# Optimization experiments

Hardware: AMD Instinct MI355X
Metric: run time of the kernel (lower is better)

The kernel has to match this reference:

```python
import jax, jax.numpy as jnp
import numpy as np

OUT_F, IN_F = 11008, 4096  # LLaMA-7B up-projection


def setup_inputs() -> dict:
    key = jax.random.key(0)
    k1, k2, k3, k4 = jax.random.split(key, 4)
    x = jax.random.normal(k1, (2, 512, IN_F), dtype=jnp.float32)
    # decoded int8 weights, stored as int32 per spec but valued in [-127, 127]
    weight_int8 = jax.random.randint(k2, (OUT_F, IN_F), -127, 128, dtype=jnp.int32)
    scale = jax.random.uniform(k3, (1,), dtype=jnp.float32) * 0.02 + 1e-3
    bias = jax.random.normal(k4, (OUT_F,), dtype=jnp.float32)
    return {"x": x, "weight_int8": weight_int8, "scale": scale, "bias": bias}


def reference(x, weight_int8, scale, bias):
    # dequantize: int8 * per-tensor scale  (done fresh every forward in original)
    weight = weight_int8.astype(jnp.float32) * scale[0]  # [out, in]
    # F.linear: x @ W^T + b
    out = jnp.einsum('bsi,oi->bso', x, weight) + bias
    return out
```

## Files before the change

kernel.cpp:

```cpp
#include <hip/hip_runtime.h>
#include <hip/hip_bf16.h>


#define M_TOT 1024
#define N_TOT 11008
#define K_TOT 4096
#define BM 256
#define BN 256
#define BKI 128
#define NTI (K_TOT / BKI)
#define ABYTES (BM * BKI)
#define BUFB   ((BM + BN) * BKI)

typedef __attribute__((ext_vector_type(8))) short short8;
typedef __attribute__((ext_vector_type(4))) float f32x4;
typedef __attribute__((ext_vector_type(4))) int   i32x4;

__device__ __forceinline__ unsigned short f2bf(float f) {
    __hip_bfloat16 h = __float2bfloat16(f);
    return __builtin_bit_cast(unsigned short, h);
}

__device__ __forceinline__ void gload16(const void* g, void* l) {
    __builtin_amdgcn_global_load_lds(
        (const __attribute__((address_space(1))) unsigned int*)g,
        (__attribute__((address_space(3))) unsigned int*)l,
        16, 0, 0);
}

__global__ void wpack_kernel(const int* __restrict__ W, int* __restrict__ Wq, int n16) {
    int idx = blockIdx.x * blockDim.x + threadIdx.x;
    int stride = gridDim.x * blockDim.x;
    for (int i = idx; i < n16; i += stride) {
        const int4* p = (const int4*)W + (size_t)i * 4;
        i32x4 o;
#pragma unroll
        for (int j = 0; j < 4; ++j) {
            int4 v = p[j];
            o[j] = (v.x & 0xff) | ((v.y & 0xff) << 8) | ((v.z & 0xff) << 16) | (v.w << 24);
        }
        *(i32x4*)(Wq + (size_t)i * 4) = o;
    }
}

__global__ __launch_bounds__(256)
void xquant_kernel(const float* __restrict__ X, int* __restrict__ Xq,
                   float* __restrict__ sx) {
    const int r = blockIdx.x;
    const int t = threadIdx.x;
    const float* xr = X + (size_t)r * K_TOT + t * 16;
    f32x4 v[4];
    float amax = 0.0f;
#pragma unroll
    for (int j = 0; j < 4; ++j) {
        v[j] = *(const f32x4*)(xr + j * 4);
#pragma unroll
        for (int e = 0; e < 4; ++e) amax = fmaxf(amax, fabsf(v[j][e]));
    }
#pragma unroll
    for (int k = 1; k < 64; k <<= 1) amax = fmaxf(amax, __shfl_xor(amax, k));
    __shared__ float sm[4];
    if ((t & 63) == 0) sm[t >> 6] = amax;
    __syncthreads();
    amax = fmaxf(fmaxf(sm[0], sm[1]), fmaxf(sm[2], sm[3]));
    const float inv = (amax > 0.0f) ? (127.0f / amax) : 0.0f;
    if (t == 0) sx[r] = (amax > 0.0f) ? (amax / 127.0f) : 0.0f;
    i32x4 o;
#pragma unroll
    for (int j = 0; j < 4; ++j) {
        int q[4];
#pragma unroll
        for (int e = 0; e < 4; ++e) {
            int qi = (int)rintf(v[j][e] * inv);
            qi = qi > 127 ? 127 : (qi < -127 ? -127 : qi);
            q[e] = qi;
        }
        o[j] = (q[0] & 0xff) | ((q[1] & 0xff) << 8) | ((q[2] & 0xff) << 16) | (q[3] << 24);
    }
    *(i32x4*)(Xq + (size_t)r * (K_TOT / 4) + t * 4) = o;
}

__global__ __launch_bounds__(512, 2)
void gemm_i8_kernel(const char* __restrict__ Xq,
                    const char* __restrict__ Wq,
                    const float* __restrict__ sx,
                    const float* __restrict__ scale,
                    const float* __restrict__ bias,
                    float* __restrict__ out) {
    __shared__ __align__(16) unsigned char lds[2 * BUFB];

    const int tid  = threadIdx.x;
    const int lane = tid & 63;
    const int wid  = tid >> 6;
    const int wr   = wid >> 2;
    const int wc   = wid & 3;
    const int lr   = lane & 15;
    const int kb   = lane >> 4;

    const int brow = blockIdx.y * BM;
    const int bcol = blockIdx.x * BN;

    const int s_row  = wid * 32 + (lane >> 3);
    const int s_colb = (((lane & 7) ^ (lane >> 3)) * 16);

    const char* asrc0 = Xq + (size_t)(brow + s_row) * K_TOT + s_colb;
    const char* bsrc0 = Wq + (size_t)(bcol + s_row) * K_TOT + s_colb;
    const int lds_row0 = wid * 32;

    auto stageA = [&](int t, unsigned char* buf) {
        const size_t k0 = (size_t)t * BKI;
#pragma unroll
        for (int i = 0; i < 4; ++i)
            gload16(asrc0 + k0 + (size_t)i * 8 * K_TOT, buf + (lds_row0 + i * 8) * BKI);
    };
    auto stageB = [&](int t, unsigned char* buf) {
        const size_t k0 = (size_t)t * BKI;
#pragma unroll
        for (int i = 0; i < 4; ++i)
            gload16(bsrc0 + k0 + (size_t)i * 8 * K_TOT, buf + ABYTES + (lds_row0 + i * 8) * BKI);
    };

    i32x4 acc[8][4];
#pragma unroll
    for (int m = 0; m < 8; ++m)
#pragma unroll
        for (int n = 0; n < 4; ++n)
#pragma unroll
            for (int i = 0; i < 4; ++i) acc[m][n][i] = 0;

    auto do_tile = [&](const unsigned char* cur, unsigned char* nxt, int tn) {
        stageA(tn, nxt);
        asm volatile("s_waitcnt vmcnt(4)" ::: "memory");
        __builtin_amdgcn_s_barrier();
        __builtin_amdgcn_sched_barrier(0);

        i32x4 a0[4], a1[4], a2[4], a3[4], b0[4], b1[4];
        const int c0 = (kb * 16);
        const int c1 = (64 + kb * 16);

#pragma unroll
        for (int n = 0; n < 4; ++n) {
            int row = wc * 64 + n * 16 + lr;
            b0[n] = *(const i32x4*)(cur + ABYTES + row * BKI + (c0 ^ ((row & 7) << 4)));
        }
#pragma unroll
        for (int m = 0; m < 4; ++m) {
            int row = wr * 128 + m * 16 + lr;
            a0[m] = *(const i32x4*)(cur + row * BKI + (c0 ^ ((row & 7) << 4)));
        }
#pragma unroll
        for (int m = 0; m < 4; ++m) {
            int row = wr * 128 + 64 + m * 16 + lr;
            a1[m] = *(const i32x4*)(cur + row * BKI + (c0 ^ ((row & 7) << 4)));
        }

        __builtin_amdgcn_s_setprio(1);
#pragma unroll
        for (int m = 0; m < 4; ++m)
#pragma unroll
            for (int n = 0; n < 4; ++n)
                acc[m][n] = __builtin_amdgcn_mfma_i32_16x16x64_i8(a0[m], b0[n], acc[m][n], 0, 0, 0);
        __builtin_amdgcn_s_setprio(0);

#pragma unroll
        for (int n = 0; n < 4; ++n) {
            int row = wc * 64 + n * 16 + lr;
            b1[n] = *(const i32x4*)(cur + ABYTES + row * BKI + (c1 ^ ((row & 7) << 4)));
        }
#pragma unroll
        for (int m = 0; m < 4; ++m) {
            int row = wr * 128 + m * 16 + lr;
            a2[m] = *(const i32x4*)(cur + row * BKI + (c1 ^ ((row & 7) << 4)));
        }

        __builtin_amdgcn_s_setprio(1);
#pragma unroll
        for (int m = 0; m < 4; ++m)
#pragma unroll
            for (int n = 0; n < 4; ++n)
                acc[4 + m][n] = __builtin_amdgcn_mfma_i32_16x16x64_i8(a1[m], b0[n], acc[4 + m][n], 0, 0, 0);
        __builtin_amdgcn_s_setprio(0);

#pragma unroll
        for (int m = 0; m < 4; ++m) {
            int row = wr * 128 + 64 + m * 16 + lr;
            a3[m] = *(const i32x4*)(cur + row * BKI + (c1 ^ ((row & 7) << 4)));
        }
        stageB(tn, nxt);

        __builtin_amdgcn_s_setprio(1);
#pragma unroll
        for (int m = 0; m < 4; ++m)
#pragma unroll
            for (int n = 0; n < 4; ++n)
                acc[m][n] = __builtin_amdgcn_mfma_i32_16x16x64_i8(a2[m], b1[n], acc[m][n], 0, 0, 0);
        __builtin_amdgcn_s_setprio(0);

        __builtin_amdgcn_s_setprio(1);
#pragma unroll
        for (int m = 0; m < 4; ++m)
#pragma unroll
            for (int n = 0; n < 4; ++n)
                acc[4 + m][n] = __builtin_amdgcn_mfma_i32_16x16x64_i8(a3[m], b1[n], acc[4 + m][n], 0, 0, 0);
        __builtin_amdgcn_s_setprio(0);

        asm volatile("s_waitcnt lgkmcnt(0)" ::: "memory");
        __builtin_amdgcn_s_barrier();
    };

    unsigned char* buf0 = lds;
    unsigned char* buf1 = lds + BUFB;

    stageA(0, buf0);
    stageB(0, buf0);

    for (int t = 0; t < NTI; t += 2) {
        do_tile(buf0, buf1, t + 1);
        do_tile(buf1, buf0, (t + 2 < NTI) ? t + 2 : 0);
    }

    const float sw = scale[0];
    const int orow0 = brow + wr * 128;
    const int ocol0 = bcol + wc * 64;
    float bv[4];
#pragma unroll
    for (int n = 0; n < 4; ++n) bv[n] = bias[ocol0 + n * 16 + lr];
#pragma unroll
    for (int m = 0; m < 8; ++m) {
        f32x4 sx4 = *(const f32x4*)(sx + orow0 + m * 16 + kb * 4);
#pragma unroll
        for (int i = 0; i < 4; ++i) {
            int r = orow0 + m * 16 + kb * 4 + i;
            size_t base = (size_t)r * N_TOT + ocol0;
            float fs = sx4[i] * sw;
#pragma unroll
            for (int n = 0; n < 4; ++n)
                out[base + n * 16 + lr] = (float)acc[m][n][i] * fs + bv[n];
        }
    }
}

__device__ __forceinline__ unsigned long long pack4(float a, float b, float c, float d) {
    return (unsigned long long)f2bf(a)
         | ((unsigned long long)f2bf(b) << 16)
         | ((unsigned long long)f2bf(c) << 32)
         | ((unsigned long long)f2bf(d) << 48);
}

#define FBM 128
#define FBN 128
#define FBK 64
#define FNT (K_TOT / FBK)

__global__ __launch_bounds__(256, 2)
void otf_linear_fused(const float* __restrict__ X, const int* __restrict__ W,
                      const float* __restrict__ scale, const float* __restrict__ bias,
                      float* __restrict__ out) {
    __shared__ __align__(16) unsigned char AsB[FBM * FBK * 2];
    __shared__ __align__(16) unsigned char BsB[FBN * FBK * 2];

    const int tid = threadIdx.x, lane = tid & 63, wid = tid >> 6;
    const int wr = wid >> 1, wc = wid & 1, lr = lane & 15, kb = lane >> 4;
    const int brow = blockIdx.y * FBM, bcol = blockIdx.x * FBN;
    const int srow = tid >> 4, sc4 = tid & 15;

    f32x4 areg[8];
    int4 breg[8];
    auto load_tiles = [&](int t) {
        const int k0 = t * FBK;
#pragma unroll
        for (int p = 0; p < 8; ++p) {
            int row = p * 16 + srow;
            areg[p] = *(const f32x4*)(&X[(size_t)(brow + row) * K_TOT + k0 + sc4 * 4]);
            breg[p] = *(const int4*)(&W[(size_t)(bcol + row) * K_TOT + k0 + sc4 * 4]);
        }
    };
    auto store_tiles = [&]() {
#pragma unroll
        for (int p = 0; p < 8; ++p) {
            int row = p * 16 + srow;
            int boff = (sc4 * 8) ^ ((row & 7) << 4);
            *(unsigned long long*)(&AsB[row * 128 + boff]) =
                pack4(areg[p][0], areg[p][1], areg[p][2], areg[p][3]);
            *(unsigned long long*)(&BsB[row * 128 + boff]) =
                pack4((float)breg[p].x, (float)breg[p].y, (float)breg[p].z, (float)breg[p].w);
        }
    };

    f32x4 acc[4][4];
#pragma unroll
    for (int m = 0; m < 4; ++m)
#pragma unroll
        for (int n = 0; n < 4; ++n)
#pragma unroll
            for (int i = 0; i < 4; ++i) acc[m][n][i] = 0.0f;

    load_tiles(0);
    for (int t = 0; t < FNT; ++t) {
        store_tiles();
        __syncthreads();
        if (t + 1 < FNT) load_tiles(t + 1);
#pragma unroll
        for (int kk = 0; kk < 2; ++kk) {
            short8 af[4], bfr[4];
#pragma unroll
            for (int m = 0; m < 4; ++m) {
                int row = wr * 64 + m * 16 + lr;
                int col = (kk * 64 + kb * 16) ^ ((row & 7) << 4);
                af[m] = *(const short8*)(&AsB[row * 128 + col]);
            }
#pragma unroll
            for (int n = 0; n < 4; ++n) {
                int row = wc * 64 + n * 16 + lr;
                int col = (kk * 64 + kb * 16) ^ ((row & 7) << 4);
                bfr[n] = *(const short8*)(&BsB[row * 128 + col]);
            }
#pragma unroll
            for (int m = 0; m < 4; ++m)
#pragma unroll
                for (int n = 0; n < 4; ++n)
                    acc[m][n] = __builtin_amdgcn_mfma_f32_16x16x32_bf16(af[m], bfr[n], acc[m][n], 0, 0, 0);
        }
        __syncthreads();
    }

    const float sc = scale[0];
    const int orow0 = brow + wr * 64, ocol0 = bcol + wc * 64;
    float bv[4];
#pragma unroll
    for (int n = 0; n < 4; ++n) bv[n] = bias[ocol0 + n * 16 + lr];
#pragma unroll
    for (int m = 0; m < 4; ++m)
#pragma unroll
        for (int i = 0; i < 4; ++i) {
            int r = orow0 + m * 16 + kb * 4 + i;
            size_t base = (size_t)r * N_TOT + ocol0;
#pragma unroll
            for (int n = 0; n < 4; ++n)
                out[base + n * 16 + lr] = acc[m][n][i] * sc + bv[n];
        }
}

extern "C" void kernel_launch(void* const* d_in, const int* in_sizes, int n_in,
                              void* d_out, int out_size, void* d_ws, size_t ws_size,
                              hipStream_t stream) {
    const float* x     = (const float*)d_in[0];
    const int*   w     = (const int*)d_in[1];
    const float* scale = (const float*)d_in[2];
    const float* bias  = (const float*)d_in[3];
    float* out = (float*)d_out;

    const size_t W_ELEMS = (size_t)N_TOT * K_TOT;
    const size_t X_ELEMS = (size_t)M_TOT * K_TOT;
    const size_t need = W_ELEMS + X_ELEMS + M_TOT * sizeof(float);

    if (ws_size >= need) {
        char*  Wq = (char*)d_ws;
        char*  Xq = (char*)d_ws + W_ELEMS;
        float* sx = (float*)((char*)d_ws + W_ELEMS + X_ELEMS);
        wpack_kernel<<<2048, 256, 0, stream>>>(w, (int*)Wq, (int)(W_ELEMS / 16));
        xquant_kernel<<<M_TOT, 256, 0, stream>>>(x, (int*)Xq, sx);
        gemm_i8_kernel<<<dim3(N_TOT / BN, M_TOT / BM), 512, 0, stream>>>(
            Xq, Wq, sx, scale, bias, out);
    } else {
        otf_linear_fused<<<dim3(N_TOT / FBN, M_TOT / FBM), 256, 0, stream>>>(x, w, scale, bias, out);
    }
}
```

Before: 96.48 us.

## Fuse int32 weight packing into the int8 GEMM with smaller tiles and XCD swizzle

Removes the separate weight-packing pass that converted the int32 weights to int8 in workspace. The GEMM now loads raw int32 weight rows into registers, packs them to int8 and writes them to LDS inside the K-loop, alongside the async LDS loads for the quantized activations. Tiles shrink from 256x256 to 128x128 with 256 threads, and a 1D grid is remapped so that blocks sharing a weight column tile land on the same XCD for L2 reuse. This saves a full read and write of the weights in an extra kernel, but the GEMM now reads four times as many weight bytes per tile. It also waits on all vector loads every tile, which may expose global-load latency.

```diff
diff --git a/kernel.cpp b/kernel.cpp
--- a/kernel.cpp
+++ b/kernel.cpp
@@ -5,12 +5,12 @@
 #define M_TOT 1024
 #define N_TOT 11008
 #define K_TOT 4096
-#define BM 256
-#define BN 256
+#define BM 128
+#define BN 128
 #define BKI 128
 #define NTI (K_TOT / BKI)
-#define ABYTES (BM * BKI)
-#define BUFB   ((BM + BN) * BKI)
+#define ABYTES_ (BM * BKI)
+#define BUFB    ((BM + BN) * BKI)
 
 typedef __attribute__((ext_vector_type(8))) short short8;
 typedef __attribute__((ext_vector_type(4))) float f32x4;
@@ -26,21 +26,6 @@
         (const __attribute__((address_space(1))) unsigned int*)g,
         (__attribute__((address_space(3))) unsigned int*)l,
         16, 0, 0);
-}
-
-__global__ void wpack_kernel(const int* __restrict__ W, int* __restrict__ Wq, int n16) {
-    int idx = blockIdx.x * blockDim.x + threadIdx.x;
-    int stride = gridDim.x * blockDim.x;
-    for (int i = idx; i < n16; i += stride) {
-        const int4* p = (const int4*)W + (size_t)i * 4;
-        i32x4 o;
-#pragma unroll
-        for (int j = 0; j < 4; ++j) {
-            int4 v = p[j];
-            o[j] = (v.x & 0xff) | ((v.y & 0xff) << 8) | ((v.z & 0xff) << 16) | (v.w << 24);
-        }
-        *(i32x4*)(Wq + (size_t)i * 4) = o;
-    }
 }
 
 __global__ __launch_bounds__(256)
@@ -80,32 +65,33 @@
     *(i32x4*)(Xq + (size_t)r * (K_TOT / 4) + t * 4) = o;
 }
 
-__global__ __launch_bounds__(512, 2)
-void gemm_i8_kernel(const char* __restrict__ Xq,
-                    const char* __restrict__ Wq,
-                    const float* __restrict__ sx,
-                    const float* __restrict__ scale,
-                    const float* __restrict__ bias,
-                    float* __restrict__ out) {
+__global__ __launch_bounds__(256, 2)
+void gemm_fused_kernel(const char* __restrict__ Xq,
+                       const int* __restrict__ W,
+                       const float* __restrict__ sx,
+                       const float* __restrict__ scale,
+                       const float* __restrict__ bias,
+                       float* __restrict__ out) {
     __shared__ __align__(16) unsigned char lds[2 * BUFB];
 
     const int tid  = threadIdx.x;
     const int lane = tid & 63;
     const int wid  = tid >> 6;
-    const int wr   = wid >> 2;
-    const int wc   = wid & 3;
+    const int wr   = wid >> 1;
+    const int wc   = wid & 1;
     const int lr   = lane & 15;
     const int kb   = lane >> 4;
 
-    const int brow = blockIdx.y * BM;
-    const int bcol = blockIdx.x * BN;
-
-    const int s_row  = wid * 32 + (lane >> 3);
-    const int s_colb = (((lane & 7) ^ (lane >> 3)) * 16);
+    const int orig = blockIdx.x;
+    const int wg   = (orig & 7) * 86 + (orig >> 3);
+    const int brow = (wg & 7) * BM;
+    const int bcol = (wg >> 3) * BN;
+
+    const int lds_row0 = wid * 32;
+    const int s_row  = lds_row0 + (lane >> 3);
+    const int s_colb = ((lane & 7) ^ (lane >> 3)) * 16;
 
     const char* asrc0 = Xq + (size_t)(brow + s_row) * K_TOT + s_colb;
-    const char* bsrc0 = Wq + (size_t)(bcol + s_row) * K_TOT + s_colb;
-    const int lds_row0 = wid * 32;
 
     auto stageA = [&](int t, unsigned char* buf) {
         const size_t k0 = (size_t)t * BKI;
@@ -113,47 +99,70 @@
         for (int i = 0; i < 4; ++i)
             gload16(asrc0 + k0 + (size_t)i * 8 * K_TOT, buf + (lds_row0 + i * 8) * BKI);
     };
-    auto stageB = [&](int t, unsigned char* buf) {
-        const size_t k0 = (size_t)t * BKI;
+
+    const int* bW[4];
+#pragma unroll
+    for (int i = 0; i < 4; ++i)
+        bW[i] = W + (size_t)(bcol + lds_row0 + i * 8 + (lane >> 3)) * K_TOT + (lane & 7) * 16;
+
+    auto packw = [&](const int4 q[4]) {
+        i32x4 o;
+#pragma unroll
+        for (int j = 0; j < 4; ++j)
+            o[j] = (q[j].x & 0xff) | ((q[j].y & 0xff) << 8) |
+                   ((q[j].z & 0xff) << 16) | (q[j].w << 24);
+        return o;
+    };
+    auto bwrite = [&](unsigned char* buf, int i, i32x4 v) {
+        *(i32x4*)(buf + ABYTES_ + (lds_row0 + i * 8 + (lane >> 3)) * BKI + s_colb) = v;
+    };
+
+    i32x4 acc[4][4];
+#pragma unroll
+    for (int m = 0; m < 4; ++m)
+#pragma unroll
+        for (int n = 0; n < 4; ++n)
+#pragma unroll
+            for (int i = 0; i < 4; ++i) acc[m][n][i] = 0;
+
+    unsigned char* buf0 = lds;
+    unsigned char* buf1 = lds + BUFB;
+
+    {
+        int4 bq[4][4];
 #pragma unroll
         for (int i = 0; i < 4; ++i)
-            gload16(bsrc0 + k0 + (size_t)i * 8 * K_TOT, buf + ABYTES + (lds_row0 + i * 8) * BKI);
-    };
-
-    i32x4 acc[8][4];
-#pragma unroll
-    for (int m = 0; m < 8; ++m)
-#pragma unroll
-        for (int n = 0; n < 4; ++n)
-#pragma unroll
-            for (int i = 0; i < 4; ++i) acc[m][n][i] = 0;
+#pragma unroll
+            for (int j = 0; j < 4; ++j)
+                bq[i][j] = *(const int4*)(bW[i] + j * 4);
+        stageA(0, buf0);
+#pragma unroll
+        for (int i = 0; i < 4; ++i) bwrite(buf0, i, packw(bq[i]));
+        asm volatile("s_waitcnt vmcnt(0) lgkmcnt(0)" ::: "memory");
+        __builtin_amdgcn_s_barrier();
+    }
 
     auto do_tile = [&](const unsigned char* cur, unsigned char* nxt, int tn) {
+        int4 bq[4][4];
+#pragma unroll
+        for (int i = 0; i < 4; ++i)
+#pragma unroll
+            for (int j = 0; j < 4; ++j)
+                bq[i][j] = *(const int4*)(bW[i] + tn * BKI + j * 4);
         stageA(tn, nxt);
-        asm volatile("s_waitcnt vmcnt(4)" ::: "memory");
-        __builtin_amdgcn_s_barrier();
         __builtin_amdgcn_sched_barrier(0);
 
-        i32x4 a0[4], a1[4], a2[4], a3[4], b0[4], b1[4];
-        const int c0 = (kb * 16);
-        const int c1 = (64 + kb * 16);
-
+        i32x4 a0[4], b0[4], a1[4], b1[4];
 #pragma unroll
         for (int n = 0; n < 4; ++n) {
             int row = wc * 64 + n * 16 + lr;
-            b0[n] = *(const i32x4*)(cur + ABYTES + row * BKI + (c0 ^ ((row & 7) << 4)));
+            b0[n] = *(const i32x4*)(cur + ABYTES_ + row * BKI + ((kb * 16) ^ ((row & 7) << 4)));
         }
 #pragma unroll
         for (int m = 0; m < 4; ++m) {
-            int row = wr * 128 + m * 16 + lr;
-            a0[m] = *(const i32x4*)(cur + row * BKI + (c0 ^ ((row & 7) << 4)));
-        }
-#pragma unroll
-        for (int m = 0; m < 4; ++m) {
-            int row = wr * 128 + 64 + m * 16 + lr;
-            a1[m] = *(const i32x4*)(cur + row * BKI + (c0 ^ ((row & 7) << 4)));
-        }
-
+            int row = wr * 64 + m * 16 + lr;
+            a0[m] = *(const i32x4*)(cur + row * BKI + ((kb * 16) ^ ((row & 7) << 4)));
+        }
         __builtin_amdgcn_s_setprio(1);
 #pragma unroll
         for (int m = 0; m < 4; ++m)
@@ -161,58 +170,35 @@
             for (int n = 0; n < 4; ++n)
                 acc[m][n] = __builtin_amdgcn_mfma_i32_16x16x64_i8(a0[m], b0[n], acc[m][n], 0, 0, 0);
         __builtin_amdgcn_s_setprio(0);
+        __builtin_amdgcn_sched_barrier(0);
+
+        bwrite(nxt, 0, packw(bq[0]));
+        bwrite(nxt, 1, packw(bq[1]));
 
 #pragma unroll
         for (int n = 0; n < 4; ++n) {
             int row = wc * 64 + n * 16 + lr;
-            b1[n] = *(const i32x4*)(cur + ABYTES + row * BKI + (c1 ^ ((row & 7) << 4)));
+            b1[n] = *(const i32x4*)(cur + ABYTES_ + row * BKI + ((64 + kb * 16) ^ ((row & 7) << 4)));
         }
 #pragma unroll
         for (int m = 0; m < 4; ++m) {
-            int row = wr * 128 + m * 16 + lr;
-            a2[m] = *(const i32x4*)(cur + row * BKI + (c1 ^ ((row & 7) << 4)));
-        }
-
+            int row = wr * 64 + m * 16 + lr;
+            a1[m] = *(const i32x4*)(cur + row * BKI + ((64 + kb * 16) ^ ((row & 7) << 4)));
+        }
         __builtin_amdgcn_s_setprio(1);
 #pragma unroll
         for (int m = 0; m < 4; ++m)
 #pragma unroll
             for (int n = 0; n < 4; ++n)
-                acc[4 + m][n] = __builtin_amdgcn_mfma_i32_16x16x64_i8(a1[m], b0[n], acc[4 + m][n], 0, 0, 0);
+                acc[m][n] = __builtin_amdgcn_mfma_i32_16x16x64_i8(a1[m], b1[n], acc[m][n], 0, 0, 0);
         __builtin_amdgcn_s_setprio(0);
 
-#pragma unroll
-        for (int m = 0; m < 4; ++m) {
-            int row = wr * 128 + 64 + m * 16 + lr;
-            a3[m] = *(const i32x4*)(cur + row * BKI + (c1 ^ ((row & 7) << 4)));
-        }
-        stageB(tn, nxt);
-
-        __builtin_amdgcn_s_setprio(1);
-#pragma unroll
-        for (int m = 0; m < 4; ++m)
-#pragma unroll
-            for (int n = 0; n < 4; ++n)
-                acc[m][n] = __builtin_amdgcn_mfma_i32_16x16x64_i8(a2[m], b1[n], acc[m][n], 0, 0, 0);
-        __builtin_amdgcn_s_setprio(0);
-
-        __builtin_amdgcn_s_setprio(1);
-#pragma unroll
-        for (int m = 0; m < 4; ++m)
-#pragma unroll
-            for (int n = 0; n < 4; ++n)
-                acc[4 + m][n] = __builtin_amdgcn_mfma_i32_16x16x64_i8(a3[m], b1[n], acc[4 + m][n], 0, 0, 0);
-        __builtin_amdgcn_s_setprio(0);
-
-        asm volatile("s_waitcnt lgkmcnt(0)" ::: "memory");
+        bwrite(nxt, 2, packw(bq[2]));
+        bwrite(nxt, 3, packw(bq[3]));
+
+        asm volatile("s_waitcnt vmcnt(0) lgkmcnt(0)" ::: "memory");
         __builtin_amdgcn_s_barrier();
     };
-
-    unsigned char* buf0 = lds;
-    unsigned char* buf1 = lds + BUFB;
-
-    stageA(0, buf0);
-    stageB(0, buf0);
 
     for (int t = 0; t < NTI; t += 2) {
         do_tile(buf0, buf1, t + 1);
@@ -220,13 +206,13 @@
     }
 
     const float sw = scale[0];
-    const int orow0 = brow + wr * 128;
+    const int orow0 = brow + wr * 64;
     const int ocol0 = bcol + wc * 64;
     float bv[4];
 #pragma unroll
     for (int n = 0; n < 4; ++n) bv[n] = bias[ocol0 + n * 16 + lr];
 #pragma unroll
-    for (int m = 0; m < 8; ++m) {
+    for (int m = 0; m < 4; ++m) {
         f32x4 sx4 = *(const f32x4*)(sx + orow0 + m * 16 + kb * 4);
 #pragma unroll
         for (int i = 0; i < 4; ++i) {
@@ -350,18 +336,14 @@
     const float* bias  = (const float*)d_in[3];
     float* out = (float*)d_out;
 
-    const size_t W_ELEMS = (size_t)N_TOT * K_TOT;
     const size_t X_ELEMS = (size_t)M_TOT * K_TOT;
-    const size_t need = W_ELEMS + X_ELEMS + M_TOT * sizeof(float);
+    const size_t need = X_ELEMS + M_TOT * sizeof(float);
 
     if (ws_size >= need) {
-        char*  Wq = (char*)d_ws;
-        char*  Xq = (char*)d_ws + W_ELEMS;
-        float* sx = (float*)((char*)d_ws + W_ELEMS + X_ELEMS);
-        wpack_kernel<<<2048, 256, 0, stream>>>(w, (int*)Wq, (int)(W_ELEMS / 16));
+        char*  Xq = (char*)d_ws;
+        float* sx = (float*)((char*)d_ws + X_ELEMS);
         xquant_kernel<<<M_TOT, 256, 0, stream>>>(x, (int*)Xq, sx);
-        gemm_i8_kernel<<<dim3(N_TOT / BN, M_TOT / BM), 512, 0, stream>>>(
-            Xq, Wq, sx, scale, bias, out);
+        gemm_fused_kernel<<<dim3(688), 256, 0, stream>>>(Xq, w, sx, scale, bias, out);
     } else {
         otf_linear_fused<<<dim3(N_TOT / FBN, M_TOT / FBM), 256, 0, stream>>>(x, w, scale, bias, out);
     }
```

Result: slower. 156.4 us (+62.1%).

## Fuse int32-to-int8 weight packing into the GEMM B-tile staging

Applied to the files above, without the earlier changes.

Removes the separate weight-packing kernel and its int8 workspace. The GEMM now reads the int32 weights straight from global memory into registers, packs them to int8 and writes them into the swizzled LDS B tile. The loads and packs are interleaved with the MFMA phases, and the end-of-tile wait now also covers outstanding global loads. This drops a full extra pass over the weights. In exchange, each row-block reads the 4-byte weights rather than packed bytes, which quadruples weight traffic unless the caches absorb it. It also adds register pressure and a less asynchronous B path.

```diff
diff --git a/kernel.cpp b/kernel.cpp
--- a/kernel.cpp
+++ b/kernel.cpp
@@ -28,19 +28,8 @@
         16, 0, 0);
 }
 
-__global__ void wpack_kernel(const int* __restrict__ W, int* __restrict__ Wq, int n16) {
-    int idx = blockIdx.x * blockDim.x + threadIdx.x;
-    int stride = gridDim.x * blockDim.x;
-    for (int i = idx; i < n16; i += stride) {
-        const int4* p = (const int4*)W + (size_t)i * 4;
-        i32x4 o;
-#pragma unroll
-        for (int j = 0; j < 4; ++j) {
-            int4 v = p[j];
-            o[j] = (v.x & 0xff) | ((v.y & 0xff) << 8) | ((v.z & 0xff) << 16) | (v.w << 24);
-        }
-        *(i32x4*)(Wq + (size_t)i * 4) = o;
-    }
+__device__ __forceinline__ int packb(int4 v) {
+    return (v.x & 0xff) | ((v.y & 0xff) << 8) | ((v.z & 0xff) << 16) | (v.w << 24);
 }
 
 __global__ __launch_bounds__(256)
@@ -81,8 +70,8 @@
 }
 
 __global__ __launch_bounds__(512, 2)
-void gemm_i8_kernel(const char* __restrict__ Xq,
-                    const char* __restrict__ Wq,
+void gemm_fw_kernel(const char* __restrict__ Xq,
+                    const int* __restrict__ W,
                     const float* __restrict__ sx,
                     const float* __restrict__ scale,
                     const float* __restrict__ bias,
@@ -99,13 +88,11 @@
 
     const int brow = blockIdx.y * BM;
     const int bcol = blockIdx.x * BN;
-
-    const int s_row  = wid * 32 + (lane >> 3);
+    const int lds_row0 = wid * 32;
+
+    const int s_row  = lds_row0 + (lane >> 3);
     const int s_colb = (((lane & 7) ^ (lane >> 3)) * 16);
-
     const char* asrc0 = Xq + (size_t)(brow + s_row) * K_TOT + s_colb;
-    const char* bsrc0 = Wq + (size_t)(bcol + s_row) * K_TOT + s_colb;
-    const int lds_row0 = wid * 32;
 
     auto stageA = [&](int t, unsigned char* buf) {
         const size_t k0 = (size_t)t * BKI;
@@ -113,11 +100,26 @@
         for (int i = 0; i < 4; ++i)
             gload16(asrc0 + k0 + (size_t)i * 8 * K_TOT, buf + (lds_row0 + i * 8) * BKI);
     };
-    auto stageB = [&](int t, unsigned char* buf) {
-        const size_t k0 = (size_t)t * BKI;
-#pragma unroll
-        for (int i = 0; i < 4; ++i)
-            gload16(bsrc0 + k0 + (size_t)i * 8 * K_TOT, buf + ABYTES + (lds_row0 + i * 8) * BKI);
+
+    const int* bW = W + (size_t)(bcol + lds_row0 + (lane >> 2)) * K_TOT + (lane & 3) * 16;
+
+    auto loadBh = [&](int t, int h, int4 r[2][4]) {
+#pragma unroll
+        for (int s = 0; s < 2; ++s)
+#pragma unroll
+            for (int j = 0; j < 4; ++j)
+                r[s][j] = *(const int4*)(bW + (size_t)s * 16 * K_TOT + t * BKI + h * 64 + j * 4);
+    };
+    auto packBh = [&](int h, const int4 r[2][4], unsigned char* buf) {
+#pragma unroll
+        for (int s = 0; s < 2; ++s) {
+            i32x4 o;
+#pragma unroll
+            for (int j = 0; j < 4; ++j) o[j] = packb(r[s][j]);
+            int row = lds_row0 + s * 16 + (lane >> 2);
+            int off = (h * 64 + (lane & 3) * 16) ^ ((row & 7) << 4);
+            *(i32x4*)(buf + ABYTES + row * BKI + off) = o;
+        }
     };
 
     i32x4 acc[8][4];
@@ -127,11 +129,23 @@
         for (int n = 0; n < 4; ++n)
 #pragma unroll
             for (int i = 0; i < 4; ++i) acc[m][n][i] = 0;
+
+    unsigned char* buf0 = lds;
+    unsigned char* buf1 = lds + BUFB;
+
+    {
+        stageA(0, buf0);
+        int4 rb[2][4];
+        loadBh(0, 0, rb); packBh(0, rb, buf0);
+        loadBh(0, 1, rb); packBh(1, rb, buf0);
+        asm volatile("s_waitcnt vmcnt(0) lgkmcnt(0)" ::: "memory");
+        __builtin_amdgcn_s_barrier();
+    }
 
     auto do_tile = [&](const unsigned char* cur, unsigned char* nxt, int tn) {
         stageA(tn, nxt);
-        asm volatile("s_waitcnt vmcnt(4)" ::: "memory");
-        __builtin_amdgcn_s_barrier();
+        int4 rb[2][4];
+        loadBh(tn, 0, rb);
         __builtin_amdgcn_sched_barrier(0);
 
         i32x4 a0[4], a1[4], a2[4], a3[4], b0[4], b1[4];
@@ -162,6 +176,9 @@
                 acc[m][n] = __builtin_amdgcn_mfma_i32_16x16x64_i8(a0[m], b0[n], acc[m][n], 0, 0, 0);
         __builtin_amdgcn_s_setprio(0);
 
+        packBh(0, rb, nxt);
+        loadBh(tn, 1, rb);
+
 #pragma unroll
         for (int n = 0; n < 4; ++n) {
             int row = wc * 64 + n * 16 + lr;
@@ -186,7 +203,6 @@
             int row = wr * 128 + 64 + m * 16 + lr;
             a3[m] = *(const i32x4*)(cur + row * BKI + (c1 ^ ((row & 7) << 4)));
         }
-        stageB(tn, nxt);
 
         __builtin_amdgcn_s_setprio(1);
 #pragma unroll
@@ -196,6 +212,8 @@
                 acc[m][n] = __builtin_amdgcn_mfma_i32_16x16x64_i8(a2[m], b1[n], acc[m][n], 0, 0, 0);
         __builtin_amdgcn_s_setprio(0);
 
+        packBh(1, rb, nxt);
+
         __builtin_amdgcn_s_setprio(1);
 #pragma unroll
         for (int m = 0; m < 4; ++m)
@@ -204,15 +222,9 @@
                 acc[4 + m][n] = __builtin_amdgcn_mfma_i32_16x16x64_i8(a3[m], b1[n], acc[4 + m][n], 0, 0, 0);
         __builtin_amdgcn_s_setprio(0);
 
-        asm volatile("s_waitcnt lgkmcnt(0)" ::: "memory");
+        asm volatile("s_waitcnt vmcnt(0) lgkmcnt(0)" ::: "memory");
         __builtin_amdgcn_s_barrier();
     };
-
-    unsigned char* buf0 = lds;
-    unsigned char* buf1 = lds + BUFB;
-
-    stageA(0, buf0);
-    stageB(0, buf0);
 
     for (int t = 0; t < NTI; t += 2) {
         do_tile(buf0, buf1, t + 1);
@@ -350,18 +362,15 @@
     const float* bias  = (const float*)d_in[3];
     float* out = (float*)d_out;
 
-    const size_t W_ELEMS = (size_t)N_TOT * K_TOT;
     const size_t X_ELEMS = (size_t)M_TOT * K_TOT;
-    const size_t need = W_ELEMS + X_ELEMS + M_TOT * sizeof(float);
+    const size_t need = X_ELEMS + M_TOT * sizeof(float);
 
     if (ws_size >= need) {
-        char*  Wq = (char*)d_ws;
-        char*  Xq = (char*)d_ws + W_ELEMS;
-        float* sx = (float*)((char*)d_ws + W_ELEMS + X_ELEMS);
-        wpack_kernel<<<2048, 256, 0, stream>>>(w, (int*)Wq, (int)(W_ELEMS / 16));
+        char*  Xq = (char*)d_ws;
+        float* sx = (float*)((char*)d_ws + X_ELEMS);
         xquant_kernel<<<M_TOT, 256, 0, stream>>>(x, (int*)Xq, sx);
-        gemm_i8_kernel<<<dim3(N_TOT / BN, M_TOT / BM), 512, 0, stream>>>(
-            Xq, Wq, sx, scale, bias, out);
+        gemm_fw_kernel<<<dim3(N_TOT / BN, M_TOT / BM), 512, 0, stream>>>(
+            Xq, w, sx, scale, bias, out);
     } else {
         otf_linear_fused<<<dim3(N_TOT / FBN, M_TOT / FBM), 256, 0, stream>>>(x, w, scale, bias, out);
     }
```

Result: slower. 137.2 us (+42.2%).
